# Kernel optimization log

Hardware: AMD Instinct MI355X
Metric: run time of the kernel (lower is better)

The kernel has to match this reference:

```python
import jax, jax.numpy as jnp
import numpy as np

V, H, B, S, J, T, NOP = 30000, 512, 16, 256, 10, 8, 4
NEG = -1e9


def setup_inputs() -> dict:
    key = jax.random.key(0)
    ks = jax.random.split(key, 10)
    return {
        "x": jax.random.randint(ks[0], (B, S), 0, V),
        "encoder_output": jax.random.normal(ks[1], (B, S, H), jnp.float32),
        "encoder_hidden": jax.random.normal(ks[2], (B, H), jnp.float32),
        "max_len": T,
        "emb_W": jax.random.normal(ks[3], (V, H), jnp.float32) * 0.02,
        "slot_emb": jax.random.normal(ks[4], (J, H), jnp.float32) * 0.1,
        "W_ih": jax.random.normal(ks[5], (3 * H, H), jnp.float32) * 0.02,
        "W_hh": jax.random.normal(ks[6], (3 * H, H), jnp.float32) * 0.02,
        "b_ih": jnp.zeros((3 * H,), jnp.float32),
        "b_hh": jnp.zeros((3 * H,), jnp.float32),
        "w_gen_W": jax.random.normal(ks[7], (1, 3 * H), jnp.float32) * 0.02,
        "w_gen_b": jnp.zeros((1,), jnp.float32),
        "action_W": jax.random.normal(ks[8], (NOP, H), jnp.float32) * 0.02,
        "action_b": jnp.zeros((NOP,), jnp.float32),
    }


def gru_step(xin, h, W_ih, W_hh, b_ih, b_hh):
    # xin, h: (J, B, H). PyTorch GRU gate order: r, z, n.
    gi = xin @ W_ih.T + b_ih
    gh = h @ W_hh.T + b_hh
    ir, iz, inn = jnp.split(gi, 3, axis=-1)
    hr, hz, hn = jnp.split(gh, 3, axis=-1)
    r = jax.nn.sigmoid(ir + hr)
    z = jax.nn.sigmoid(iz + hz)
    n = jnp.tanh(inn + r * hn)
    return (1.0 - z) * n + z * h


def reference(x, encoder_output, encoder_hidden, max_len, emb_W, slot_emb,
              W_ih, W_hh, b_ih, b_hh, w_gen_W, w_gen_b, action_W, action_b):
    nJ, nH = slot_emb.shape
    nB, nS = x.shape
    nV = emb_W.shape[0]
    mask = (x == 0)  # (B, S) pad mask
    xJ = jnp.broadcast_to(x[None], (nJ, nB, nS))
    jidx = jnp.arange(nJ)[:, None, None]
    bidx = jnp.arange(nB)[None, :, None]

    w0 = jnp.broadcast_to(slot_emb[:, None, :], (nJ, nB, nH))  # slot query per slot
    h0 = jnp.broadcast_to(encoder_hidden[None], (nJ, nB, nH))

    def step(carry, _):
        w, h = carry
        h = gru_step(w, h, W_ih, W_hh, b_ih, b_hh)
        # attention over encoder states
        attn_e = jnp.einsum('bsh,jbh->jbs', encoder_output, h)
        attn_e = jnp.where(mask[None], NEG, attn_e)
        attn_hist = jax.nn.softmax(attn_e, axis=-1)          # (J,B,S)
        context = jnp.einsum('jbs,bsh->jbh', attn_hist, encoder_output)
        # vocab distribution
        attn_vocab = jax.nn.softmax(h @ emb_W.T, axis=-1)    # (J,B,V)
        # pointer-generator mix
        gen_in = jnp.concatenate([w, h, context], axis=-1)   # (J,B,3H)
        p_gen = jax.nn.sigmoid(gen_in @ w_gen_W.T + w_gen_b) # (J,B,1)
        p_ctx = jnp.zeros((nJ, nB, nV), attn_vocab.dtype).at[jidx, bidx, xJ].add(attn_hist)
        p_final = p_gen * attn_vocab + (1.0 - p_gen) * p_ctx # (J,B,V)
        w_idx = jnp.argmax(p_final, axis=-1)                 # greedy next token
        w_next = emb_W[w_idx]                                # (J,B,H)
        return (w_next, h), (p_final, context)

    (_, _), (p_all, ctx_all) = jax.lax.scan(step, (w0, h0), None, length=max_len)
    # gate head uses context from first decode step (k == 0)
    gates = ctx_all[0] @ action_W.T + action_b               # (J,B,n_op)
    all_gate = jnp.transpose(gates, (1, 0, 2))               # (B,J,n_op)
    all_point = jnp.transpose(p_all, (2, 1, 0, 3))           # (B,J,T,V)
    return all_gate, all_point
```

## Files before the change

kernel.cpp:

```cpp
#include <hip/hip_runtime.h>
#include <math.h>

#define V 30000
#define H 512
#define NB 16
#define NS 256
#define NJ 10
#define NT 8
#define NOPS 4
#define NR 160
#define EV 30720
#define NEGV -1e9f

typedef __attribute__((ext_vector_type(8))) short short8;
typedef __attribute__((ext_vector_type(4))) short short4v;
typedef __attribute__((ext_vector_type(4))) float f32x4;

__device__ inline float bf2f(unsigned short s) {
    union { unsigned int u; float f; } c; c.u = ((unsigned int)s) << 16;
    return c.f;
}
__device__ inline unsigned short f2bf(float f) {
    union { float f; unsigned int u; } c; c.f = f;
    unsigned int u = c.u;
    u += 0x7fffu + ((u >> 16) & 1u);
    return (unsigned short)(u >> 16);
}
__device__ inline unsigned long long packkey(float f, int v) {
    union { float f; unsigned int u; } c; c.f = f;
    return ((unsigned long long)c.u << 32) | (unsigned int)(0x7FFFFFFF - v);
}

__global__ void k_setup_emb(const float* __restrict__ emb, unsigned short* __restrict__ emb_bf, int n8) {
    int gid = blockIdx.x * 256 + threadIdx.x;
    if (gid >= n8) return;
    const float4* src = (const float4*)emb + (size_t)gid * 2;
    float4 a = src[0], b = src[1];
    short8 o;
    o[0] = (short)f2bf(a.x); o[1] = (short)f2bf(a.y); o[2] = (short)f2bf(a.z); o[3] = (short)f2bf(a.w);
    o[4] = (short)f2bf(b.x); o[5] = (short)f2bf(b.y); o[6] = (short)f2bf(b.z); o[7] = (short)f2bf(b.w);
    *(short8*)(emb_bf + (size_t)gid * 8) = o;
}

__global__ void k_setup_small(const float* __restrict__ Wih, const float* __restrict__ Whh,
    unsigned short* wih_hi, unsigned short* wih_lo, unsigned short* whh_hi, unsigned short* whh_lo,
    const float* __restrict__ slot, const float* __restrict__ ench,
    float* w_g, unsigned short* w_hi, unsigned short* w_lo,
    float* h_g, unsigned short* h_hi, unsigned short* h_lo)
{
    int gid = blockIdx.x * 256 + threadIdx.x;
    if (gid < 786432) {
        float v1 = Wih[gid];
        unsigned short hi = f2bf(v1);
        wih_hi[gid] = hi; wih_lo[gid] = f2bf(v1 - bf2f(hi));
        float v2 = Whh[gid];
        hi = f2bf(v2);
        whh_hi[gid] = hi; whh_lo[gid] = f2bf(v2 - bf2f(hi));
    } else {
        int i = gid - 786432;
        if (i < NR * H) {
            int jb = i >> 9, d = i & 511;
            int j = jb >> 4, b = jb & 15;
            float wv = slot[j * H + d];
            w_g[i] = wv;
            unsigned short hi = f2bf(wv);
            w_hi[i] = hi; w_lo[i] = f2bf(wv - bf2f(hi));
            float hv = ench[b * H + d];
            h_g[i] = hv;
            hi = f2bf(hv);
            h_hi[i] = hi; h_lo[i] = f2bf(hv - bf2f(hi));
        }
    }
}

#define GRU_APAD 520
__global__ __launch_bounds__(256) void k_gru_gemm(
    const unsigned short* __restrict__ w_hi, const unsigned short* __restrict__ w_lo,
    const unsigned short* __restrict__ h_hi, const unsigned short* __restrict__ h_lo,
    const unsigned short* __restrict__ wih_hi, const unsigned short* __restrict__ wih_lo,
    const unsigned short* __restrict__ whh_hi, const unsigned short* __restrict__ whh_lo,
    float* __restrict__ gi, float* __restrict__ gh)
{
    __shared__ unsigned short Ah[16 * GRU_APAD];
    __shared__ unsigned short Al[16 * GRU_APAD];
    int nch = blockIdx.x, mt = blockIdx.y, z = blockIdx.z;
    const unsigned short* Asrc_hi = z ? h_hi : w_hi;
    const unsigned short* Asrc_lo = z ? h_lo : w_lo;
    const unsigned short* Bhi = z ? whh_hi : wih_hi;
    const unsigned short* Blo = z ? whh_lo : wih_lo;
    float* outp = z ? gh : gi;
    int t = threadIdx.x;
    for (int i = t; i < 2048; i += 256) {
        int matl = i >> 10;
        int row = (i >> 6) & 15;
        int seg = i & 63;
        const unsigned short* src = (matl ? Asrc_lo : Asrc_hi) + (mt * 16 + row) * 512 + seg * 8;
        unsigned short* dst = (matl ? Al : Ah) + row * GRU_APAD + seg * 8;
        *(short8*)dst = *(const short8*)src;
    }
    __syncthreads();
    int wv = t >> 6, lane = t & 63;
    int col15 = lane & 15, quad = lane >> 4;
    f32x4 acc0 = {0.f, 0.f, 0.f, 0.f}, acc1 = {0.f, 0.f, 0.f, 0.f};
    int c0 = nch * 128 + wv * 32 + col15;
    int c1 = c0 + 16;
    const unsigned short* bhp0 = Bhi + c0 * 512 + quad * 8;
    const unsigned short* bhp1 = Bhi + c1 * 512 + quad * 8;
    const unsigned short* blp0 = Blo + c0 * 512 + quad * 8;
    const unsigned short* blp1 = Blo + c1 * 512 + quad * 8;
    const unsigned short* ahp = Ah + col15 * GRU_APAD + quad * 8;
    const unsigned short* alp = Al + col15 * GRU_APAD + quad * 8;
#pragma unroll
    for (int ks = 0; ks < 16; ks++) {
        int ko = ks * 32;
        short8 bh0 = *(const short8*)(bhp0 + ko);
        short8 bh1 = *(const short8*)(bhp1 + ko);
        short8 bl0 = *(const short8*)(blp0 + ko);
        short8 bl1 = *(const short8*)(blp1 + ko);
        short8 ah = *(const short8*)(ahp + ko);
        short8 al = *(const short8*)(alp + ko);
        acc0 = __builtin_amdgcn_mfma_f32_16x16x32_bf16(ah, bh0, acc0, 0, 0, 0);
        acc1 = __builtin_amdgcn_mfma_f32_16x16x32_bf16(ah, bh1, acc1, 0, 0, 0);
        acc0 = __builtin_amdgcn_mfma_f32_16x16x32_bf16(ah, bl0, acc0, 0, 0, 0);
        acc1 = __builtin_amdgcn_mfma_f32_16x16x32_bf16(ah, bl1, acc1, 0, 0, 0);
        acc0 = __builtin_amdgcn_mfma_f32_16x16x32_bf16(al, bh0, acc0, 0, 0, 0);
        acc1 = __builtin_amdgcn_mfma_f32_16x16x32_bf16(al, bh1, acc1, 0, 0, 0);
    }
#pragma unroll
    for (int r = 0; r < 4; r++) {
        int row = mt * 16 + quad * 4 + r;
        outp[row * 1536 + c0] = acc0[r];
        outp[row * 1536 + c1] = acc1[r];
    }
}

__global__ __launch_bounds__(256) void k_attention(
    const float* __restrict__ gi, const float* __restrict__ gh,
    const float* __restrict__ b_ih, const float* __restrict__ b_hh,
    float* __restrict__ h_g, unsigned short* __restrict__ h_hi, unsigned short* __restrict__ h_lo,
    const float* __restrict__ enc, const int* __restrict__ x,
    const float* __restrict__ w_g, const float* __restrict__ wgenW, const float* __restrict__ wgenb,
    float* __restrict__ attn_g, float* __restrict__ pgen_g,
    float* __restrict__ ctx0, int store_ctx,
    float* __restrict__ rowsum, unsigned long long* __restrict__ argpk)
{
    __shared__ float h_lds[512];
    __shared__ float sc[256];
    __shared__ float red[256];
    __shared__ float ctxp[4 * 512];
    int jb = blockIdx.x;
    int b = jb & 15;
    int t = threadIdx.x;
    if (t == 0) { rowsum[jb] = 0.f; argpk[jb] = 0ull; }
    for (int d = t; d < 512; d += 256) {
        int base = jb * 1536;
        float ir = gi[base + d]        + b_ih[d];
        float iz = gi[base + 512 + d]  + b_ih[512 + d];
        float in = gi[base + 1024 + d] + b_ih[1024 + d];
        float hr = gh[base + d]        + b_hh[d];
        float hz = gh[base + 512 + d]  + b_hh[512 + d];
        float hn = gh[base + 1024 + d] + b_hh[1024 + d];
        float hold = h_g[jb * 512 + d];
        float r = 1.f / (1.f + expf(-(ir + hr)));
        float z = 1.f / (1.f + expf(-(iz + hz)));
        float n = tanhf(in + r * hn);
        float hnew = (1.f - z) * n + z * hold;
        h_lds[d] = hnew;
        h_g[jb * 512 + d] = hnew;
        unsigned short hi = f2bf(hnew);
        h_hi[jb * 512 + d] = hi;
        h_lo[jb * 512 + d] = f2bf(hnew - bf2f(hi));
    }
    __syncthreads();
    int wid = t >> 6, lane = t & 63;
    float hreg[8];
#pragma unroll
    for (int i = 0; i < 8; i++) hreg[i] = h_lds[lane * 8 + i];
    const float* encb = enc + (size_t)b * NS * H;
    for (int s = wid; s < NS; s += 4) {
        const float4* er = (const float4*)(encb + s * 512 + lane * 8);
        float4 e0 = er[0], e1 = er[1];
        float p = e0.x * hreg[0] + e0.y * hreg[1] + e0.z * hreg[2] + e0.w * hreg[3]
                + e1.x * hreg[4] + e1.y * hreg[5] + e1.z * hreg[6] + e1.w * hreg[7];
#pragma unroll
        for (int off = 32; off > 0; off >>= 1) p += __shfl_down(p, off);
        if (lane == 0) sc[s] = (x[b * NS + s] == 0) ? NEGV : p;
    }
    __syncthreads();
    red[t] = sc[t];
    __syncthreads();
    for (int sft = 128; sft > 0; sft >>= 1) { if (t < sft) red[t] = fmaxf(red[t], red[t + sft]); __syncthreads(); }
    float m = red[0];
    __syncthreads();
    float e = expf(sc[t] - m);
    red[t] = e;
    __syncthreads();
    for (int sft = 128; sft > 0; sft >>= 1) { if (t < sft) red[t] += red[t + sft]; __syncthreads(); }
    float inv = 1.f / red[0];
    float p_s = e * inv;
    sc[t] = p_s;
    attn_g[jb * NS + t] = p_s;
    __syncthreads();
    {
        float cp[8] = {0.f,0.f,0.f,0.f,0.f,0.f,0.f,0.f};
        const float* encw = encb + lane * 8;
        for (int s = wid * 64; s < wid * 64 + 64; s++) {
            float ps = sc[s];
            const float4* er = (const float4*)(encw + s * 512);
            float4 e0 = er[0], e1 = er[1];
            cp[0] += ps * e0.x; cp[1] += ps * e0.y; cp[2] += ps * e0.z; cp[3] += ps * e0.w;
            cp[4] += ps * e1.x; cp[5] += ps * e1.y; cp[6] += ps * e1.z; cp[7] += ps * e1.w;
        }
        float* cw = ctxp + wid * 512 + lane * 8;
#pragma unroll
        for (int i = 0; i < 8; i++) cw[i] = cp[i];
    }
    __syncthreads();
    int d0 = 2 * t, d1 = 2 * t + 1;
    float c0 = ctxp[d0] + ctxp[512 + d0] + ctxp[1024 + d0] + ctxp[1536 + d0];
    float c1 = ctxp[d1] + ctxp[512 + d1] + ctxp[1024 + d1] + ctxp[1536 + d1];
    if (store_ctx) ((float2*)ctx0)[jb * 256 + t] = make_float2(c0, c1);
    float pg = wgenW[d0] * w_g[jb * 512 + d0] + wgenW[d1] * w_g[jb * 512 + d1]
             + wgenW[512 + d0] * h_lds[d0] + wgenW[512 + d1] * h_lds[d1]
             + wgenW[1024 + d0] * c0 + wgenW[1024 + d1] * c1;
    __syncthreads();
    red[t] = pg;
    __syncthreads();
    for (int sft = 128; sft > 0; sft >>= 1) { if (t < sft) red[t] += red[t + sft]; __syncthreads(); }
    if (t == 0) pgen_g[jb] = 1.f / (1.f + expf(-(red[0] + wgenb[0])));
}

#define VPAD 136
__global__ __launch_bounds__(256) void k_vgemm(
    const unsigned short* __restrict__ h_hi, const unsigned short* __restrict__ emb_bf,
    unsigned short* __restrict__ E, float* __restrict__ rowsum,
    unsigned long long* __restrict__ argpk)
{
    __shared__ unsigned short A[160 * VPAD];
    int blk = blockIdx.x;
    int t = threadIdx.x;
    int wv = t >> 6, lane = t & 63, col15 = lane & 15, quad = lane >> 4;
    int v = blk * 128 + wv * 32 + col15;
    f32x4 acc[10][2];
#pragma unroll
    for (int m = 0; m < 10; m++) {
        acc[m][0] = (f32x4){0.f, 0.f, 0.f, 0.f};
        acc[m][1] = (f32x4){0.f, 0.f, 0.f, 0.f};
    }
    int v0c = min(v, V - 1);
    int v1c = min(v + 16, V - 1);
    for (int kc = 0; kc < 4; kc++) {
        __syncthreads();
        for (int i = t; i < 2560; i += 256) {
            int row = i >> 4, seg = i & 15;
            *(short8*)(A + row * VPAD + seg * 8) = *(const short8*)(h_hi + row * 512 + kc * 128 + seg * 8);
        }
        __syncthreads();
#pragma unroll
        for (int ks = 0; ks < 4; ks++) {
            int kl = ks * 32 + quad * 8;
            int kg = kc * 128 + kl;
            short8 b0 = *(const short8*)(emb_bf + (size_t)v0c * 512 + kg);
            short8 b1 = *(const short8*)(emb_bf + (size_t)v1c * 512 + kg);
#pragma unroll
            for (int m = 0; m < 10; m++) {
                short8 a = *(const short8*)(A + (m * 16 + col15) * VPAD + kl);
                acc[m][0] = __builtin_amdgcn_mfma_f32_16x16x32_bf16(a, b0, acc[m][0], 0, 0, 0);
                acc[m][1] = __builtin_amdgcn_mfma_f32_16x16x32_bf16(a, b1, acc[m][1], 0, 0, 0);
            }
        }
    }
    __syncthreads();
#pragma unroll
    for (int m = 0; m < 10; m++) {
#pragma unroll
        for (int tile = 0; tile < 2; tile++) {
            int vv = v + tile * 16;
            int cl = wv * 32 + tile * 16 + col15;
#pragma unroll
            for (int r = 0; r < 4; r++) {
                int row = m * 16 + quad * 4 + r;
                float ev = (vv < V) ? expf(acc[m][tile][r]) : 0.f;
                A[row * VPAD + cl] = f2bf(ev);
            }
        }
    }
    __syncthreads();
    if (t < 160) {
        float s = 0.f;
        unsigned long long key = 0ull;
#pragma unroll
        for (int seg = 0; seg < 16; seg++) {
            short8 ev = *(const short8*)(A + t * VPAD + seg * 8);
#pragma unroll
            for (int k = 0; k < 8; k++) {
                float f = bf2f((unsigned short)ev[k]);
                s += f;
                unsigned long long kk = packkey(f, blk * 128 + seg * 8 + k);
                key = (kk > key) ? kk : key;
            }
        }
        atomicAdd(rowsum + t, s);
        atomicMax(argpk + t, key);
    }
    {
        int rsub = t >> 4, seg = t & 15;
        for (int it = 0; it < 10; it++) {
            int row = it * 16 + rsub;
            short8 ev = *(const short8*)(A + row * VPAD + seg * 8);
            *(short8*)(E + (size_t)row * EV + blk * 128 + seg * 8) = ev;
        }
    }
}

__global__ __launch_bounds__(256) void k_finalize(
    const unsigned short* __restrict__ E, const float* __restrict__ pgen_g,
    const float* __restrict__ rowsum, const unsigned long long* __restrict__ argpk,
    const float* __restrict__ attn_g, const int* __restrict__ x,
    const float* __restrict__ emb, float* __restrict__ out,
    float* __restrict__ w_g, unsigned short* __restrict__ w_hi, unsigned short* __restrict__ w_lo,
    const float* __restrict__ ctx0, const float* __restrict__ aW, const float* __restrict__ ab,
    int tstep)
{
    __shared__ float bvs[256];
    __shared__ int bis[256];
    __shared__ float red[256];
    int jb = blockIdx.x, t = threadIdx.x;
    int j = jb >> 4, b = jb & 15;
    float inv = 1.f / rowsum[jb];
    float pgen = pgen_g[jb];
    float scale = pgen * inv;
    const unsigned short* Er = E + (size_t)jb * EV;
    size_t outbase = (size_t)640 + ((size_t)(b * NJ + j) * NT + tstep) * V;
    float* op = out + outbase;
    for (int c = 0; c < 29; c++) {
        int vv = c * 1024 + t * 4;
        short4v e = *(const short4v*)(Er + vv);
        float4 p = make_float4(bf2f((unsigned short)e[0]) * scale, bf2f((unsigned short)e[1]) * scale,
                               bf2f((unsigned short)e[2]) * scale, bf2f((unsigned short)e[3]) * scale);
        *(float4*)(op + vv) = p;
    }
    if (t < 76) {
        int vv = 29696 + t * 4;
        short4v e = *(const short4v*)(Er + vv);
        float4 p = make_float4(bf2f((unsigned short)e[0]) * scale, bf2f((unsigned short)e[1]) * scale,
                               bf2f((unsigned short)e[2]) * scale, bf2f((unsigned short)e[3]) * scale);
        *(float4*)(op + vv) = p;
    }
    __syncthreads();
    float best; int besti;
    {
        int vv = x[b * NS + t];
        float a = (1.f - pgen) * attn_g[jb * NS + t];
        float old = atomicAdd(&op[vv], a);
        best = old + a;
        besti = vv;
    }
    bvs[t] = best; bis[t] = besti;
    __syncthreads();
    for (int sft = 128; sft > 0; sft >>= 1) {
        if (t < sft) {
            if (bvs[t + sft] > bvs[t] || (bvs[t + sft] == bvs[t] && bis[t + sft] < bis[t])) {
                bvs[t] = bvs[t + sft]; bis[t] = bis[t + sft];
            }
        }
        __syncthreads();
    }
    int widx;
    {
        unsigned long long key = argpk[jb];
        union { unsigned int u; float f; } c; c.u = (unsigned int)(key >> 32);
        float db = c.f * scale;
        int di = 0x7FFFFFFF - (int)(key & 0xFFFFFFFFu);
        float sb = bvs[0]; int si = bis[0];
        widx = (sb > db || (sb == db && si < di)) ? si : di;
    }
    for (int d = t; d < 512; d += 256) {
        float val = emb[(size_t)widx * 512 + d];
        w_g[jb * 512 + d] = val;
        unsigned short hi = f2bf(val);
        w_hi[jb * 512 + d] = hi;
        w_lo[jb * 512 + d] = f2bf(val - bf2f(hi));
    }
    if (tstep == 0) {
        float part[4] = {0.f, 0.f, 0.f, 0.f};
        for (int d = t; d < 512; d += 256) {
            float c = ctx0[jb * 512 + d];
#pragma unroll
            for (int o = 0; o < 4; o++) part[o] += c * aW[o * 512 + d];
        }
        for (int o = 0; o < 4; o++) {
            __syncthreads();
            red[t] = part[o];
            __syncthreads();
            for (int sft = 128; sft > 0; sft >>= 1) { if (t < sft) red[t] += red[t + sft]; __syncthreads(); }
            if (t == 0) out[(b * NJ + j) * NOPS + o] = red[0] + ab[o];
        }
    }
}

extern "C" void kernel_launch(void* const* d_in, const int* in_sizes, int n_in,
                              void* d_out, int out_size, void* d_ws, size_t ws_size,
                              hipStream_t stream) {
    const int*   x     = (const int*)d_in[0];
    const float* enc   = (const float*)d_in[1];
    const float* ench  = (const float*)d_in[2];
    const float* embW  = (const float*)d_in[4];
    const float* slot  = (const float*)d_in[5];
    const float* Wih   = (const float*)d_in[6];
    const float* Whh   = (const float*)d_in[7];
    const float* bih   = (const float*)d_in[8];
    const float* bhh   = (const float*)d_in[9];
    const float* wgenW = (const float*)d_in[10];
    const float* wgenb = (const float*)d_in[11];
    const float* aW    = (const float*)d_in[12];
    const float* ab    = (const float*)d_in[13];
    float* out = (float*)d_out;

    char* ws = (char*)d_ws;
    size_t off = 0;
    auto carve = [&](size_t bytes) { char* p = ws + off; off += (bytes + 255) & ~(size_t)255; return p; };
    unsigned short* emb_bf = (unsigned short*)carve((size_t)V * H * 2);
    unsigned short* wih_hi = (unsigned short*)carve(786432 * 2);
    unsigned short* wih_lo = (unsigned short*)carve(786432 * 2);
    unsigned short* whh_hi = (unsigned short*)carve(786432 * 2);
    unsigned short* whh_lo = (unsigned short*)carve(786432 * 2);
    float* w_f32 = (float*)carve(NR * H * 4);
    float* h_f32 = (float*)carve(NR * H * 4);
    float* ctx0  = (float*)carve(NR * H * 4);
    unsigned short* w_hi = (unsigned short*)carve(NR * H * 2);
    unsigned short* w_lo = (unsigned short*)carve(NR * H * 2);
    unsigned short* h_hi = (unsigned short*)carve(NR * H * 2);
    unsigned short* h_lo = (unsigned short*)carve(NR * H * 2);
    float* gi   = (float*)carve(NR * 1536 * 4);
    float* gh   = (float*)carve(NR * 1536 * 4);
    float* attn = (float*)carve(NR * NS * 4);
    float* pgen = (float*)carve(NR * 4);
    float* rowsum = (float*)carve(NR * 4);
    unsigned long long* argpk = (unsigned long long*)carve(NR * 8);
    unsigned short* E = (unsigned short*)carve((size_t)NR * EV * 2);

    k_setup_emb<<<7500, 256, 0, stream>>>(embW, emb_bf, (V * H) / 8);
    k_setup_small<<<3392, 256, 0, stream>>>(Wih, Whh, wih_hi, wih_lo, whh_hi, whh_lo,
                                            slot, ench, w_f32, w_hi, w_lo, h_f32, h_hi, h_lo);
    for (int t = 0; t < NT; t++) {
        k_gru_gemm<<<dim3(12, 10, 2), 256, 0, stream>>>(w_hi, w_lo, h_hi, h_lo,
                                                        wih_hi, wih_lo, whh_hi, whh_lo, gi, gh);
        k_attention<<<NR, 256, 0, stream>>>(gi, gh, bih, bhh, h_f32, h_hi, h_lo, enc, x,
                                            w_f32, wgenW, wgenb, attn, pgen, ctx0, t == 0 ? 1 : 0,
                                            rowsum, argpk);
        k_vgemm<<<240, 256, 0, stream>>>(h_hi, emb_bf, E, rowsum, argpk);
        k_finalize<<<NR, 256, 0, stream>>>(E, pgen, rowsum, argpk, attn, x, embW, out,
                                           w_f32, w_hi, w_lo, ctx0, aW, ab, t);
    }
}
```

Before: 1.100 ms.

## Pre-pack embedding and hidden state into MFMA fragment layout for vocab GEMM

Embedding weights are converted to bf16 once and stored in the per-lane MFMA fragment order, so each lane in the vocab GEMM loads a contiguous 16-byte chunk instead of gathering strided rows. The hidden state is also written in packed fragment order by setup and attention, which lets the GEMM stage A into shared memory with contiguous copies and read it conflict-free. The finalize loop is widened to 8-element loads and stores. In exchange, setup does an extra LDS transpose, and attention performs an additional scattered write per element.

```diff
diff --git a/kernel.cpp b/kernel.cpp
--- a/kernel.cpp
+++ b/kernel.cpp
@@ -11,6 +11,7 @@
 #define NR 160
 #define EV 30720
 #define NEGV -1e9f
+#define NTILES 1875
 
 typedef __attribute__((ext_vector_type(8))) short short8;
 typedef __attribute__((ext_vector_type(4))) short short4v;
@@ -31,22 +32,38 @@
     return ((unsigned long long)c.u << 32) | (unsigned int)(0x7FFFFFFF - v);
 }
 
-__global__ void k_setup_emb(const float* __restrict__ emb, unsigned short* __restrict__ emb_bf, int n8) {
-    int gid = blockIdx.x * 256 + threadIdx.x;
-    if (gid >= n8) return;
-    const float4* src = (const float4*)emb + (size_t)gid * 2;
-    float4 a = src[0], b = src[1];
-    short8 o;
-    o[0] = (short)f2bf(a.x); o[1] = (short)f2bf(a.y); o[2] = (short)f2bf(a.z); o[3] = (short)f2bf(a.w);
-    o[4] = (short)f2bf(b.x); o[5] = (short)f2bf(b.y); o[6] = (short)f2bf(b.z); o[7] = (short)f2bf(b.w);
-    *(short8*)(emb_bf + (size_t)gid * 8) = o;
+__global__ __launch_bounds__(256) void k_setup_pack(const float* __restrict__ emb,
+                                                    unsigned short* __restrict__ emb_pk) {
+    __shared__ unsigned short L[16 * 512];
+    int nt = blockIdx.x;
+    int t = threadIdx.x;
+#pragma unroll
+    for (int i = 0; i < 4; i++) {
+        int o = i * 2048 + t * 8;
+        int row = o >> 9, k = o & 511;
+        const float4* src = (const float4*)(emb + (size_t)(nt * 16 + row) * 512 + k);
+        float4 a = src[0], b = src[1];
+        short8 v;
+        v[0] = (short)f2bf(a.x); v[1] = (short)f2bf(a.y); v[2] = (short)f2bf(a.z); v[3] = (short)f2bf(a.w);
+        v[4] = (short)f2bf(b.x); v[5] = (short)f2bf(b.y); v[6] = (short)f2bf(b.z); v[7] = (short)f2bf(b.w);
+        *(short8*)(L + o) = v;
+    }
+    __syncthreads();
+#pragma unroll
+    for (int i = 0; i < 4; i++) {
+        int idx = i * 256 + t;
+        int ks = idx >> 6, l = idx & 63;
+        int col15 = l & 15, quad = l >> 4;
+        short8 v = *(const short8*)(L + col15 * 512 + ks * 32 + quad * 8);
+        *(short8*)(emb_pk + ((size_t)(nt * 16 + ks) * 64 + l) * 8) = v;
+    }
 }
 
 __global__ void k_setup_small(const float* __restrict__ Wih, const float* __restrict__ Whh,
     unsigned short* wih_hi, unsigned short* wih_lo, unsigned short* whh_hi, unsigned short* whh_lo,
     const float* __restrict__ slot, const float* __restrict__ ench,
     float* w_g, unsigned short* w_hi, unsigned short* w_lo,
-    float* h_g, unsigned short* h_hi, unsigned short* h_lo)
+    float* h_g, unsigned short* h_hi, unsigned short* h_lo, unsigned short* h_pk)
 {
     int gid = blockIdx.x * 256 + threadIdx.x;
     if (gid < 786432) {
@@ -69,6 +86,8 @@
             h_g[i] = hv;
             hi = f2bf(hv);
             h_hi[i] = hi; h_lo[i] = f2bf(hv - bf2f(hi));
+            int ks = d >> 5, quad = (d >> 3) & 3, e = d & 7;
+            h_pk[(((jb >> 4) * 16 + ks) * 64 + quad * 16 + (jb & 15)) * 8 + e] = hi;
         }
     }
 }
@@ -138,6 +157,7 @@
     const float* __restrict__ gi, const float* __restrict__ gh,
     const float* __restrict__ b_ih, const float* __restrict__ b_hh,
     float* __restrict__ h_g, unsigned short* __restrict__ h_hi, unsigned short* __restrict__ h_lo,
+    unsigned short* __restrict__ h_pk,
     const float* __restrict__ enc, const int* __restrict__ x,
     const float* __restrict__ w_g, const float* __restrict__ wgenW, const float* __restrict__ wgenb,
     float* __restrict__ attn_g, float* __restrict__ pgen_g,
@@ -152,6 +172,7 @@
     int b = jb & 15;
     int t = threadIdx.x;
     if (t == 0) { rowsum[jb] = 0.f; argpk[jb] = 0ull; }
+    int m_pk = jb >> 4, c_pk = jb & 15;
     for (int d = t; d < 512; d += 256) {
         int base = jb * 1536;
         float ir = gi[base + d]        + b_ih[d];
@@ -170,6 +191,8 @@
         unsigned short hi = f2bf(hnew);
         h_hi[jb * 512 + d] = hi;
         h_lo[jb * 512 + d] = f2bf(hnew - bf2f(hi));
+        int ks = d >> 5, quad = (d >> 3) & 3, e = d & 7;
+        h_pk[((m_pk * 16 + ks) * 64 + quad * 16 + c_pk) * 8 + e] = hi;
     }
     __syncthreads();
     int wid = t >> 6, lane = t & 63;
@@ -232,7 +255,7 @@
 
 #define VPAD 136
 __global__ __launch_bounds__(256) void k_vgemm(
-    const unsigned short* __restrict__ h_hi, const unsigned short* __restrict__ emb_bf,
+    const unsigned short* __restrict__ h_pk, const unsigned short* __restrict__ emb_pk,
     unsigned short* __restrict__ E, float* __restrict__ rowsum,
     unsigned long long* __restrict__ argpk)
 {
@@ -240,31 +263,33 @@
     int blk = blockIdx.x;
     int t = threadIdx.x;
     int wv = t >> 6, lane = t & 63, col15 = lane & 15, quad = lane >> 4;
-    int v = blk * 128 + wv * 32 + col15;
     f32x4 acc[10][2];
 #pragma unroll
     for (int m = 0; m < 10; m++) {
         acc[m][0] = (f32x4){0.f, 0.f, 0.f, 0.f};
         acc[m][1] = (f32x4){0.f, 0.f, 0.f, 0.f};
     }
-    int v0c = min(v, V - 1);
-    int v1c = min(v + 16, V - 1);
+    int nt0 = blk * 8 + wv * 2;
+    int nt0c = min(nt0, NTILES - 1);
+    int nt1c = min(nt0 + 1, NTILES - 1);
     for (int kc = 0; kc < 4; kc++) {
         __syncthreads();
-        for (int i = t; i < 2560; i += 256) {
-            int row = i >> 4, seg = i & 15;
-            *(short8*)(A + row * VPAD + seg * 8) = *(const short8*)(h_hi + row * 512 + kc * 128 + seg * 8);
+#pragma unroll
+        for (int i = 0; i < 10; i++) {
+            int o = i * 2048 + t * 8;
+            int m = o >> 11, rem = o & 2047;
+            *(short8*)(A + m * 2048 + rem) =
+                *(const short8*)(h_pk + (size_t)(m * 16 + kc * 4) * 512 + rem);
         }
         __syncthreads();
 #pragma unroll
-        for (int ks = 0; ks < 4; ks++) {
-            int kl = ks * 32 + quad * 8;
-            int kg = kc * 128 + kl;
-            short8 b0 = *(const short8*)(emb_bf + (size_t)v0c * 512 + kg);
-            short8 b1 = *(const short8*)(emb_bf + (size_t)v1c * 512 + kg);
+        for (int q = 0; q < 4; q++) {
+            int ksg = kc * 4 + q;
+            short8 b0 = *(const short8*)(emb_pk + ((size_t)(nt0c * 16 + ksg) * 64 + lane) * 8);
+            short8 b1 = *(const short8*)(emb_pk + ((size_t)(nt1c * 16 + ksg) * 64 + lane) * 8);
 #pragma unroll
             for (int m = 0; m < 10; m++) {
-                short8 a = *(const short8*)(A + (m * 16 + col15) * VPAD + kl);
+                short8 a = *(const short8*)(A + m * 2048 + q * 512 + lane * 8);
                 acc[m][0] = __builtin_amdgcn_mfma_f32_16x16x32_bf16(a, b0, acc[m][0], 0, 0, 0);
                 acc[m][1] = __builtin_amdgcn_mfma_f32_16x16x32_bf16(a, b1, acc[m][1], 0, 0, 0);
             }
@@ -275,8 +300,8 @@
     for (int m = 0; m < 10; m++) {
 #pragma unroll
         for (int tile = 0; tile < 2; tile++) {
-            int vv = v + tile * 16;
             int cl = wv * 32 + tile * 16 + col15;
+            int vv = blk * 128 + cl;
 #pragma unroll
             for (int r = 0; r < 4; r++) {
                 int row = m * 16 + quad * 4 + r;
@@ -333,19 +358,25 @@
     const unsigned short* Er = E + (size_t)jb * EV;
     size_t outbase = (size_t)640 + ((size_t)(b * NJ + j) * NT + tstep) * V;
     float* op = out + outbase;
-    for (int c = 0; c < 29; c++) {
-        int vv = c * 1024 + t * 4;
-        short4v e = *(const short4v*)(Er + vv);
-        float4 p = make_float4(bf2f((unsigned short)e[0]) * scale, bf2f((unsigned short)e[1]) * scale,
-                               bf2f((unsigned short)e[2]) * scale, bf2f((unsigned short)e[3]) * scale);
-        *(float4*)(op + vv) = p;
-    }
-    if (t < 76) {
-        int vv = 29696 + t * 4;
-        short4v e = *(const short4v*)(Er + vv);
-        float4 p = make_float4(bf2f((unsigned short)e[0]) * scale, bf2f((unsigned short)e[1]) * scale,
-                               bf2f((unsigned short)e[2]) * scale, bf2f((unsigned short)e[3]) * scale);
-        *(float4*)(op + vv) = p;
+    for (int c = 0; c < 14; c++) {
+        int vv = c * 2048 + t * 8;
+        short8 e = *(const short8*)(Er + vv);
+        float4 p0 = make_float4(bf2f((unsigned short)e[0]) * scale, bf2f((unsigned short)e[1]) * scale,
+                                bf2f((unsigned short)e[2]) * scale, bf2f((unsigned short)e[3]) * scale);
+        float4 p1 = make_float4(bf2f((unsigned short)e[4]) * scale, bf2f((unsigned short)e[5]) * scale,
+                                bf2f((unsigned short)e[6]) * scale, bf2f((unsigned short)e[7]) * scale);
+        *(float4*)(op + vv) = p0;
+        *(float4*)(op + vv + 4) = p1;
+    }
+    if (t < 166) {
+        int vv = 28672 + t * 8;
+        short8 e = *(const short8*)(Er + vv);
+        float4 p0 = make_float4(bf2f((unsigned short)e[0]) * scale, bf2f((unsigned short)e[1]) * scale,
+                                bf2f((unsigned short)e[2]) * scale, bf2f((unsigned short)e[3]) * scale);
+        float4 p1 = make_float4(bf2f((unsigned short)e[4]) * scale, bf2f((unsigned short)e[5]) * scale,
+                                bf2f((unsigned short)e[6]) * scale, bf2f((unsigned short)e[7]) * scale);
+        *(float4*)(op + vv) = p0;
+        *(float4*)(op + vv + 4) = p1;
     }
     __syncthreads();
     float best; int besti;
@@ -420,7 +451,7 @@
     char* ws = (char*)d_ws;
     size_t off = 0;
     auto carve = [&](size_t bytes) { char* p = ws + off; off += (bytes + 255) & ~(size_t)255; return p; };
-    unsigned short* emb_bf = (unsigned short*)carve((size_t)V * H * 2);
+    unsigned short* emb_pk = (unsigned short*)carve((size_t)V * H * 2);
     unsigned short* wih_hi = (unsigned short*)carve(786432 * 2);
     unsigned short* wih_lo = (unsigned short*)carve(786432 * 2);
     unsigned short* whh_hi = (unsigned short*)carve(786432 * 2);
@@ -432,6 +463,7 @@
     unsigned short* w_lo = (unsigned short*)carve(NR * H * 2);
     unsigned short* h_hi = (unsigned short*)carve(NR * H * 2);
     unsigned short* h_lo = (unsigned short*)carve(NR * H * 2);
+    unsigned short* h_pk = (unsigned short*)carve(NR * H * 2);
     float* gi   = (float*)carve(NR * 1536 * 4);
     float* gh   = (float*)carve(NR * 1536 * 4);
     float* attn = (float*)carve(NR * NS * 4);
@@ -440,16 +472,16 @@
     unsigned long long* argpk = (unsigned long long*)carve(NR * 8);
     unsigned short* E = (unsigned short*)carve((size_t)NR * EV * 2);
 
-    k_setup_emb<<<7500, 256, 0, stream>>>(embW, emb_bf, (V * H) / 8);
+    k_setup_pack<<<NTILES, 256, 0, stream>>>(embW, emb_pk);
     k_setup_small<<<3392, 256, 0, stream>>>(Wih, Whh, wih_hi, wih_lo, whh_hi, whh_lo,
-                                            slot, ench, w_f32, w_hi, w_lo, h_f32, h_hi, h_lo);
+                                            slot, ench, w_f32, w_hi, w_lo, h_f32, h_hi, h_lo, h_pk);
     for (int t = 0; t < NT; t++) {
         k_gru_gemm<<<dim3(12, 10, 2), 256, 0, stream>>>(w_hi, w_lo, h_hi, h_lo,
                                                         wih_hi, wih_lo, whh_hi, whh_lo, gi, gh);
-        k_attention<<<NR, 256, 0, stream>>>(gi, gh, bih, bhh, h_f32, h_hi, h_lo, enc, x,
+        k_attention<<<NR, 256, 0, stream>>>(gi, gh, bih, bhh, h_f32, h_hi, h_lo, h_pk, enc, x,
                                             w_f32, wgenW, wgenb, attn, pgen, ctx0, t == 0 ? 1 : 0,
                                             rowsum, argpk);
-        k_vgemm<<<240, 256, 0, stream>>>(h_hi, emb_bf, E, rowsum, argpk);
+        k_vgemm<<<235, 256, 0, stream>>>(h_pk, emb_pk, E, rowsum, argpk);
         k_finalize<<<NR, 256, 0, stream>>>(E, pgen, rowsum, argpk, attn, x, embW, out,
                                            w_f32, w_hi, w_lo, ctx0, aW, ab, t);
     }
```

New measurement: 1.113 ms. Within noise of the previous version (+1.2%).
